# Optimization experiments

Hardware: AMD Instinct MI355X
Metric: run time of the kernel (lower is better)

## Reference

```python
import jax, jax.numpy as jnp
import numpy as np

N_NODES, N_EDGES, DIM = 50000, 800000, 128


def setup_inputs() -> dict:
    key = jax.random.key(0)
    ks = jax.random.split(key, 16)
    s = 1.0 / np.sqrt(DIM)
    inp = {
        "x": jax.random.normal(ks[0], (N_NODES, DIM), dtype=jnp.float32),
        "edge_index": jax.random.randint(ks[1], (2, N_EDGES), 0, N_NODES, dtype=jnp.int64),
    }
    # 3 GIN layers, each with a 2-layer MLP (Linear-ReLU-Linear)
    for i in range(3):
        inp[f"w1_{i}"] = jax.random.normal(ks[2 + 4 * i], (DIM, DIM), dtype=jnp.float32) * s
        inp[f"b1_{i}"] = jnp.zeros((DIM,), dtype=jnp.float32)
        inp[f"w2_{i}"] = jax.random.normal(ks[3 + 4 * i], (DIM, DIM), dtype=jnp.float32) * s
        inp[f"b2_{i}"] = jnp.zeros((DIM,), dtype=jnp.float32)
    inp["wh"] = jax.random.normal(ks[14], (DIM, DIM), dtype=jnp.float32) * s
    inp["bh"] = jnp.zeros((DIM,), dtype=jnp.float32)
    return inp


def _gin_layer(h, src, dst, w1, b1, w2, b2, residual):
    # message passing: gather x[src], scatter-add at dst (aggr='sum')
    neigh = jax.ops.segment_sum(h[src], dst, num_segments=h.shape[0])
    out = h + neigh  # (1 + eps) * x + neigh, eps = 0
    out = jnp.maximum(out @ w1 + b1, 0.0) @ w2 + b2  # MLP (dropout p=0)
    if residual:  # res_fc is Identity since in_dim == out_dim
        out = out + h
    return out


def reference(x, edge_index, w1_0, b1_0, w2_0, b2_0, w1_1, b1_1, w2_1, b2_1,
              w1_2, b1_2, w2_2, b2_2, wh, bh):
    src, dst = edge_index[0], edge_index[1]
    h = x
    h = _gin_layer(h, src, dst, w1_0, b1_0, w2_0, b2_0, residual=True)
    h = _gin_layer(h, src, dst, w1_1, b1_1, w2_1, b2_1, residual=True)
    # last layer: encoding=False -> no residual
    h = _gin_layer(h, src, dst, w1_2, b1_2, w2_2, b2_2, residual=False)
    # extra_output_fc head
    return h @ wh + bh
```

## Files before the change

kernel.cpp:

```cpp
#include <hip/hip_runtime.h>
#include <hip/hip_fp16.h>

#define N_NODES 50000
#define N_EDGES 800000
#define DIM 128
#define FEAT_ELEMS (N_NODES * DIM)
#define STRIDE 64
#define NB 391
#define BCAP 3072

typedef __attribute__((ext_vector_type(8))) _Float16 f16x8;
typedef __attribute__((ext_vector_type(4))) float f32x4;
typedef __attribute__((ext_vector_type(2))) float f32x2;

#define MFMA_F16 __builtin_amdgcn_mfma_f32_16x16x32_f16


__global__ __launch_bounds__(256) void prep_combo_kernel(
    const float* __restrict__ w0, const float* __restrict__ w1,
    const float* __restrict__ w2, const float* __restrict__ w3,
    const float* __restrict__ w4, const float* __restrict__ w5,
    const float* __restrict__ w6, __half* __restrict__ dst,
    const float* __restrict__ x, __half* __restrict__ hm,
    unsigned char* __restrict__ qx, unsigned char* __restrict__ q1,
    unsigned char* __restrict__ q0, int* __restrict__ gcnt) {
    const int b = blockIdx.x;
    if (b < 112) {
        const int wsel = b >> 4;
        const int chunk = b & 15;
        const float* W;
        switch (wsel) {
            case 0: W = w0; break;
            case 1: W = w1; break;
            case 2: W = w2; break;
            case 3: W = w3; break;
            case 4: W = w4; break;
            case 5: W = w5; break;
            default: W = w6; break;
        }
        __half* d = dst + (size_t)wsel * 16384;
        int idx = chunk * 1024 + threadIdx.x;
#pragma unroll
        for (int t = 0; t < 4; ++t, idx += 256) {
            int k = idx >> 7, n = idx & 127;
            int ks = k >> 5, q = (k >> 3) & 3, j = k & 7;
            int ct = n >> 4, c = n & 15;
            int lane = q * 16 + c;
            int base = ((ks * 8 + ct) * 64 + lane) * 8 + j;
            d[base] = __float2half(W[idx]);
        }
    } else if (b < 1136) {
        int i = (b - 112) * 256 + threadIdx.x;
        const int stride = 1024 * 256;
        const int n4 = FEAT_ELEMS / 4;
        for (; i < n4; i += stride) {
            float4 v = ((const float4*)x)[i];
            __half2 h0 = __floats2half2_rn(v.x, v.y);
            __half2 h1 = __floats2half2_rn(v.z, v.w);
            uint2 u;
            u.x = *(unsigned*)&h0;
            u.y = *(unsigned*)&h1;
            ((uint2*)hm)[i] = u;
            int p = __builtin_amdgcn_cvt_pk_fp8_f32(v.x, v.y, 0, false);
            p = __builtin_amdgcn_cvt_pk_fp8_f32(v.z, v.w, p, true);
            ((int*)qx)[i] = p;
        }
    } else {
        for (int i = threadIdx.x; i < NB; i += 256) gcnt[i] = 0;
        if (threadIdx.x < 32) {
            ((unsigned*)(qx + FEAT_ELEMS))[threadIdx.x] = 0;
            ((unsigned*)(q1 + FEAT_ELEMS))[threadIdx.x] = 0;
            ((unsigned*)(q0 + FEAT_ELEMS))[threadIdx.x] = 0;
        }
    }
}


__global__ __launch_bounds__(256) void bucket_kernel(const int* __restrict__ ei,
                                                     int* __restrict__ gcnt,
                                                     long long* __restrict__ ebuf) {
    __shared__ int hist[NB];
    __shared__ int base[NB];
    __shared__ int sh_is64;
    const int tid = threadIdx.x;
    for (int i = tid; i < NB; i += 256) hist[i] = 0;
    if (tid == 0) {
        int o = 0;
        for (int i = 1; i < 64; i += 2) o |= ei[i];
        sh_is64 = (o == 0) ? 1 : 0;
    }
    __syncthreads();
    const int e0 = blockIdx.x * 2048;
    const int is64 = sh_is64;
    int sv[8], dv[8];
    int nl = 0;
#pragma unroll
    for (int k = 0; k < 8; ++k) {
        int e = e0 + k * 256 + tid;
        if (e < N_EDGES) {
            int s = is64 ? ei[2 * e] : ei[e];
            int d = is64 ? ei[2 * (N_EDGES + e)] : ei[N_EDGES + e];
            sv[nl] = s;
            dv[nl] = d;
            atomicAdd(&hist[d >> 7], 1);
            ++nl;
        }
    }
    __syncthreads();
    for (int i = tid; i < NB; i += 256) {
        int h = hist[i];
        base[i] = h ? atomicAdd(&gcnt[i], h) : 0;
    }
    __syncthreads();
    for (int i = tid; i < NB; i += 256) hist[i] = 0;
    __syncthreads();
    for (int k = 0; k < nl; ++k) {
        int b = dv[k] >> 7;
        int r = base[b] + atomicAdd(&hist[b], 1);
        if (r < BCAP)
            ebuf[(size_t)b * BCAP + r] = ((long long)sv[k] << 32) | (unsigned)dv[k];
    }
}


__global__ __launch_bounds__(256) void build_kernel(const int* __restrict__ gcnt,
                                                    const long long* __restrict__ ebuf,
                                                    int* __restrict__ cnt,
                                                    int* __restrict__ col_idx) {
    __shared__ int cur[128];
    const int b = blockIdx.x;
    const int tid = threadIdx.x;
    if (tid < 128) cur[tid] = 0;
    __syncthreads();
    int n = gcnt[b];
    if (n > BCAP) n = BCAP;
    const long long* eb = ebuf + (size_t)b * BCAP;
    for (int i = tid; i < n; i += 256) {
        long long p = eb[i];
        int d = (int)(p & 0xFFFFFFFFll);
        int s = (int)(p >> 32);
        int slot = atomicAdd(&cur[d & 127], 1);
        if (slot < STRIDE) col_idx[d * STRIDE + slot] = s;
    }
    __syncthreads();
    int node = b * 128 + tid;
    if (tid < 128 && node < N_NODES) {
        int c = cur[tid];
        if (c > STRIDE) c = STRIDE;
        const int p = (c + 7) & ~7;
        for (int s = c; s < p; ++s) col_idx[node * STRIDE + s] = N_NODES;
        cnt[node] = p;
    }
}


template <bool LAST>
__global__ __launch_bounds__(128, 4) void gin_layer_kernel(
    const __half* __restrict__ Hs,
    const unsigned char* __restrict__ Qm,
    const int* __restrict__ cnt,
    const int* __restrict__ col_idx,
    const __half* __restrict__ W1f,
    const __half* __restrict__ W2f,
    const __half* __restrict__ Whf,
    const float* __restrict__ b1,
    const float* __restrict__ b2,
    const float* __restrict__ bh,
    __half* __restrict__ Hout,
    unsigned char* __restrict__ Qout,
    float* __restrict__ Cout) {
    __shared__ __align__(16) __half tl[2048];
    __shared__ __align__(16) __half ul[2048];
    const int tid = threadIdx.x;
    const int lane = tid & 63;
    const int wid = tid >> 6;
    const int c = lane & 15;
    const int q = lane >> 4;
    const int R = blockIdx.x * 16;

    {
        const int g = tid >> 4;
        const int d0 = (tid & 15) * 8;
#define ACCQ(U)                                                             \
    {                                                                       \
        f32x2 g0 = __builtin_amdgcn_cvt_pk_f32_fp8((int)(U).x, false);      \
        f32x2 g1 = __builtin_amdgcn_cvt_pk_f32_fp8((int)(U).x, true);       \
        f32x2 g2 = __builtin_amdgcn_cvt_pk_f32_fp8((int)(U).y, false);      \
        f32x2 g3 = __builtin_amdgcn_cvt_pk_f32_fp8((int)(U).y, true);       \
        acc[0] += g0.x; acc[1] += g0.y; acc[2] += g1.x; acc[3] += g1.y;     \
        acc[4] += g2.x; acc[5] += g2.y; acc[6] += g3.x; acc[7] += g3.y;     \
    }
#pragma unroll
        for (int it = 0; it < 2; ++it) {
            const int rl = it * 8 + g;
            const size_t grow = (size_t)(R + rl);
            float acc[8];
            {
                uint4 sv = *(const uint4*)(Hs + grow * DIM + d0);
                const __half2* sp = (const __half2*)&sv;
                float2 s0 = __half22float2(sp[0]), s1 = __half22float2(sp[1]);
                float2 s2 = __half22float2(sp[2]), s3 = __half22float2(sp[3]);
                acc[0] = s0.x; acc[1] = s0.y; acc[2] = s1.x; acc[3] = s1.y;
                acc[4] = s2.x; acc[5] = s2.y; acc[6] = s3.x; acc[7] = s3.y;
            }
            const int d = cnt[grow];
            const int* ci = col_idx + grow * STRIDE;
            for (int j = 0; j < d; j += 8) {
                int4 ia = *(const int4*)(ci + j);
                int4 ib = *(const int4*)(ci + j + 4);
                uint2 u0 = *(const uint2*)(Qm + (size_t)ia.x * DIM + d0);
                uint2 u1 = *(const uint2*)(Qm + (size_t)ia.y * DIM + d0);
                uint2 u2 = *(const uint2*)(Qm + (size_t)ia.z * DIM + d0);
                uint2 u3 = *(const uint2*)(Qm + (size_t)ia.w * DIM + d0);
                uint2 u4 = *(const uint2*)(Qm + (size_t)ib.x * DIM + d0);
                uint2 u5 = *(const uint2*)(Qm + (size_t)ib.y * DIM + d0);
                uint2 u6 = *(const uint2*)(Qm + (size_t)ib.z * DIM + d0);
                uint2 u7 = *(const uint2*)(Qm + (size_t)ib.w * DIM + d0);
                ACCQ(u0) ACCQ(u1) ACCQ(u2) ACCQ(u3)
                ACCQ(u4) ACCQ(u5) ACCQ(u6) ACCQ(u7)
            }
            uint4 o;
            __half2* op = (__half2*)&o;
            op[0] = __floats2half2_rn(acc[0], acc[1]);
            op[1] = __floats2half2_rn(acc[2], acc[3]);
            op[2] = __floats2half2_rn(acc[4], acc[5]);
            op[3] = __floats2half2_rn(acc[6], acc[7]);
            *(uint4*)&tl[rl * 128 + (d0 ^ ((rl & 7) << 3))] = o;
        }
#undef ACCQ
    }
    __syncthreads();

    f16x8 a[4];
#pragma unroll
    for (int ks = 0; ks < 4; ++ks)
        a[ks] = *(const f16x8*)&tl[c * 128 + ((ks * 32 + q * 8) ^ ((c & 7) << 3))];

    f32x4 acc1[4];
#pragma unroll
    for (int t = 0; t < 4; ++t) acc1[t] = (f32x4){0.f, 0.f, 0.f, 0.f};
#pragma unroll
    for (int ks = 0; ks < 4; ++ks) {
#pragma unroll
        for (int t = 0; t < 4; ++t) {
            const int ctg = wid * 4 + t;
            f16x8 b = *(const f16x8*)(W1f + (ks * 8 + ctg) * 512 + lane * 8);
            acc1[t] = MFMA_F16(a[ks], b, acc1[t], 0, 0, 0);
        }
    }

#pragma unroll
    for (int t = 0; t < 4; ++t) {
        const int col = (wid * 4 + t) * 16 + c;
        const float bv = b1[col];
#pragma unroll
        for (int rr = 0; rr < 4; ++rr) {
            const int rl = q * 4 + rr;
            ul[rl * 128 + (col ^ ((rl & 7) << 3))] =
                __float2half(fmaxf(acc1[t][rr] + bv, 0.f));
        }
    }
    __syncthreads();

    f32x4 acc2[4];
#pragma unroll
    for (int t = 0; t < 4; ++t) acc2[t] = (f32x4){0.f, 0.f, 0.f, 0.f};
#pragma unroll
    for (int ks = 0; ks < 4; ++ks) {
        f16x8 ua = *(const f16x8*)&ul[c * 128 + ((ks * 32 + q * 8) ^ ((c & 7) << 3))];
#pragma unroll
        for (int t = 0; t < 4; ++t) {
            const int ctg = wid * 4 + t;
            f16x8 b = *(const f16x8*)(W2f + (ks * 8 + ctg) * 512 + lane * 8);
            acc2[t] = MFMA_F16(ua, b, acc2[t], 0, 0, 0);
        }
    }

#pragma unroll
    for (int t = 0; t < 4; ++t) {
        const int col = (wid * 4 + t) * 16 + c;
        const float bv = b2[col];
#pragma unroll
        for (int rr = 0; rr < 4; ++rr) {
            const int rl = q * 4 + rr;
            tl[rl * 128 + (col ^ (q << 4))] = __float2half(acc2[t][rr] + bv);
        }
    }
    __syncthreads();

    if (!LAST) {
        const int row2 = tid >> 3;
        const int cb = (tid & 7) * 8;
        const size_t grow = (size_t)(R + row2);
#pragma unroll
        for (int k = 0; k < 2; ++k) {
            const int c0 = cb + k * 64;
            uint4 hv = *(uint4*)&tl[row2 * 128 + (c0 ^ ((row2 >> 2) << 4))];
            const __half2* hp = (const __half2*)&hv;
            float2 t0 = __half22float2(hp[0]), t1 = __half22float2(hp[1]);
            float2 t2 = __half22float2(hp[2]), t3 = __half22float2(hp[3]);
            float f0 = t0.x, f1 = t0.y, f2 = t1.x, f3 = t1.y;
            float f4 = t2.x, f5 = t2.y, f6 = t3.x, f7 = t3.y;
            {
                uint4 rv = *(const uint4*)(Hs + grow * DIM + c0);
                const __half2* rp = (const __half2*)&rv;
                float2 r0 = __half22float2(rp[0]), r1 = __half22float2(rp[1]);
                float2 r2 = __half22float2(rp[2]), r3 = __half22float2(rp[3]);
                f0 += r0.x; f1 += r0.y; f2 += r1.x; f3 += r1.y;
                f4 += r2.x; f5 += r2.y; f6 += r3.x; f7 += r3.y;
            }
            uint4 ov;
            __half2* op = (__half2*)&ov;
            op[0] = __floats2half2_rn(f0, f1);
            op[1] = __floats2half2_rn(f2, f3);
            op[2] = __floats2half2_rn(f4, f5);
            op[3] = __floats2half2_rn(f6, f7);
            *(uint4*)(Hout + grow * DIM + c0) = ov;
            int q0 = __builtin_amdgcn_cvt_pk_fp8_f32(f0, f1, 0, false);
            q0 = __builtin_amdgcn_cvt_pk_fp8_f32(f2, f3, q0, true);
            int q1 = __builtin_amdgcn_cvt_pk_fp8_f32(f4, f5, 0, false);
            q1 = __builtin_amdgcn_cvt_pk_fp8_f32(f6, f7, q1, true);
            uint2 qv;
            qv.x = (unsigned)q0;
            qv.y = (unsigned)q1;
            *(uint2*)(Qout + grow * DIM + c0) = qv;
        }
    } else {
        f32x4 acc3[4];
#pragma unroll
        for (int t = 0; t < 4; ++t) acc3[t] = (f32x4){0.f, 0.f, 0.f, 0.f};
#pragma unroll
        for (int ks = 0; ks < 4; ++ks) {
            f16x8 ha =
                *(const f16x8*)&tl[c * 128 + ((ks * 32 + q * 8) ^ ((c >> 2) << 4))];
#pragma unroll
            for (int t = 0; t < 4; ++t) {
                const int ctg = wid * 4 + t;
                f16x8 b = *(const f16x8*)(Whf + (ks * 8 + ctg) * 512 + lane * 8);
                acc3[t] = MFMA_F16(ha, b, acc3[t], 0, 0, 0);
            }
        }
#pragma unroll
        for (int t = 0; t < 4; ++t) {
            const int col = (wid * 4 + t) * 16 + c;
            const float bv = bh[col];
#pragma unroll
            for (int rr = 0; rr < 4; ++rr) {
                const int row = R + q * 4 + rr;
                Cout[(size_t)row * DIM + col] = acc3[t][rr] + bv;
            }
        }
    }
}


extern "C" void kernel_launch(void* const* d_in, const int* in_sizes, int n_in,
                              void* d_out, int out_size, void* d_ws, size_t ws_size,
                              hipStream_t stream) {
    const float* x = (const float*)d_in[0];
    const int* ei = (const int*)d_in[1];
    const float* w1[3] = {(const float*)d_in[2], (const float*)d_in[6], (const float*)d_in[10]};
    const float* b1[3] = {(const float*)d_in[3], (const float*)d_in[7], (const float*)d_in[11]};
    const float* w2[3] = {(const float*)d_in[4], (const float*)d_in[8], (const float*)d_in[12]};
    const float* b2[3] = {(const float*)d_in[5], (const float*)d_in[9], (const float*)d_in[13]};
    const float* wh = (const float*)d_in[14];
    const float* bh = (const float*)d_in[15];
    float* out = (float*)d_out;

    char* ws = (char*)d_ws;
    const size_t HFEAT = (size_t)FEAT_ELEMS * sizeof(__half);
    const size_t QFEAT = (size_t)FEAT_ELEMS + 256;
    size_t off = 0;
    int* cnt = (int*)(ws + off);                         off += 200704;
    int* col_idx = (int*)(ws + off);                     off += (size_t)N_NODES * STRIDE * 4;
    int* gcnt = (int*)(ws + off);                        off += 4096;
    __half* Wf = (__half*)(ws + off);                    off += 7 * 32768;
    long long* ebuf = (long long*)(ws + off);            off += (size_t)NB * BCAP * 8;
    __half* HMx = (__half*)(ws + off);                   off += HFEAT;
    __half* HM1 = (__half*)(ws + off);                   off += HFEAT;
    __half* HM0 = (__half*)(ws + off);                   off += HFEAT;
    unsigned char* Qx = (unsigned char*)(ws + off);      off += QFEAT;
    unsigned char* Q1 = (unsigned char*)(ws + off);      off += QFEAT;
    unsigned char* Q0 = (unsigned char*)(ws + off);      off += QFEAT;

    const int GIN_BLKS = N_NODES / 16;

    prep_combo_kernel<<<1137, 256, 0, stream>>>(w1[0], w2[0], w1[1], w2[1], w1[2], w2[2],
                                                wh, Wf, x, HMx, Qx, Q1, Q0, gcnt);
    bucket_kernel<<<NB, 256, 0, stream>>>(ei, gcnt, ebuf);
    build_kernel<<<NB, 256, 0, stream>>>(gcnt, ebuf, cnt, col_idx);

#define WF(i) (Wf + (size_t)(i) * 16384)

    gin_layer_kernel<false><<<GIN_BLKS, 128, 0, stream>>>(
        HMx, Qx, cnt, col_idx, WF(0), WF(1), nullptr, b1[0], b2[0], nullptr,
        HM1, Q1, nullptr);

    gin_layer_kernel<false><<<GIN_BLKS, 128, 0, stream>>>(
        HM1, Q1, cnt, col_idx, WF(2), WF(3), nullptr, b1[1], b2[1], nullptr,
        HM0, Q0, nullptr);

    gin_layer_kernel<true><<<GIN_BLKS, 128, 0, stream>>>(
        HM0, Q0, cnt, col_idx, WF(4), WF(5), WF(6), b1[2], b2[2], bh,
        nullptr, nullptr, out);
#undef WF
}
```

Baseline: 216.2 us.

## Split fp8 feature table into column halves and fuse bucketing into prep

Stores the fp8 gather table as two 64-column halves so each aggregation pass gathers from a 3.2MB array that is more likely to stay cache-resident. The gather runs two passes, one per half, with 8 threads per row instead of 16. Edge bucketing is folded into the prep kernel, and the gcnt reset moves to a memset, which removes one kernel launch. The cost is reading col_idx twice per row and a memset node. The gcnt reset must finish before the fused kernel's atomics, which stream ordering guarantees.

```diff
diff --git a/kernel.cpp b/kernel.cpp
--- a/kernel.cpp
+++ b/kernel.cpp
@@ -16,15 +16,22 @@
 #define MFMA_F16 __builtin_amdgcn_mfma_f32_16x16x32_f16
 
 
-__global__ __launch_bounds__(256) void prep_combo_kernel(
+__global__ __launch_bounds__(256) void prep_bucket_kernel(
     const float* __restrict__ w0, const float* __restrict__ w1,
     const float* __restrict__ w2, const float* __restrict__ w3,
     const float* __restrict__ w4, const float* __restrict__ w5,
     const float* __restrict__ w6, __half* __restrict__ dst,
     const float* __restrict__ x, __half* __restrict__ hm,
-    unsigned char* __restrict__ qx, unsigned char* __restrict__ q1,
-    unsigned char* __restrict__ q0, int* __restrict__ gcnt) {
+    unsigned char* __restrict__ qxlo, unsigned char* __restrict__ qxhi,
+    unsigned char* __restrict__ q1lo, unsigned char* __restrict__ q1hi,
+    unsigned char* __restrict__ q0lo, unsigned char* __restrict__ q0hi,
+    const int* __restrict__ ei, int* __restrict__ gcnt,
+    long long* __restrict__ ebuf) {
+    __shared__ int hist[NB];
+    __shared__ int base[NB];
+    __shared__ int sh_is64;
     const int b = blockIdx.x;
+    const int tid = threadIdx.x;
     if (b < 112) {
         const int wsel = b >> 4;
         const int chunk = b & 15;
@@ -39,18 +46,18 @@
             default: W = w6; break;
         }
         __half* d = dst + (size_t)wsel * 16384;
-        int idx = chunk * 1024 + threadIdx.x;
+        int idx = chunk * 1024 + tid;
 #pragma unroll
         for (int t = 0; t < 4; ++t, idx += 256) {
             int k = idx >> 7, n = idx & 127;
             int ks = k >> 5, q = (k >> 3) & 3, j = k & 7;
             int ct = n >> 4, c = n & 15;
             int lane = q * 16 + c;
-            int base = ((ks * 8 + ct) * 64 + lane) * 8 + j;
-            d[base] = __float2half(W[idx]);
+            int bas = ((ks * 8 + ct) * 64 + lane) * 8 + j;
+            d[bas] = __float2half(W[idx]);
         }
     } else if (b < 1136) {
-        int i = (b - 112) * 256 + threadIdx.x;
+        int i = (b - 112) * 256 + tid;
         const int stride = 1024 * 256;
         const int n4 = FEAT_ELEMS / 4;
         for (; i < n4; i += stride) {
@@ -63,62 +70,58 @@
             ((uint2*)hm)[i] = u;
             int p = __builtin_amdgcn_cvt_pk_fp8_f32(v.x, v.y, 0, false);
             p = __builtin_amdgcn_cvt_pk_fp8_f32(v.z, v.w, p, true);
-            ((int*)qx)[i] = p;
+            const int node = i >> 5;
+            const int within = (i & 31) * 4;
+            if (within < 64)
+                *(int*)(qxlo + (size_t)node * 64 + within) = p;
+            else
+                *(int*)(qxhi + (size_t)node * 64 + (within - 64)) = p;
+        }
+    } else if (b < 1527) {
+        for (int i = tid; i < NB; i += 256) hist[i] = 0;
+        if (tid == 0) {
+            int o = 0;
+            for (int i = 1; i < 64; i += 2) o |= ei[i];
+            sh_is64 = (o == 0) ? 1 : 0;
+        }
+        __syncthreads();
+        const int e0 = (b - 1136) * 2048;
+        const int is64 = sh_is64;
+        int sv[8], dv[8];
+        int nl = 0;
+#pragma unroll
+        for (int k = 0; k < 8; ++k) {
+            int e = e0 + k * 256 + tid;
+            if (e < N_EDGES) {
+                int s = is64 ? ei[2 * e] : ei[e];
+                int d = is64 ? ei[2 * (N_EDGES + e)] : ei[N_EDGES + e];
+                sv[nl] = s;
+                dv[nl] = d;
+                atomicAdd(&hist[d >> 7], 1);
+                ++nl;
+            }
+        }
+        __syncthreads();
+        for (int i = tid; i < NB; i += 256) {
+            int h = hist[i];
+            base[i] = h ? atomicAdd(&gcnt[i], h) : 0;
+        }
+        __syncthreads();
+        for (int i = tid; i < NB; i += 256) hist[i] = 0;
+        __syncthreads();
+        for (int k = 0; k < nl; ++k) {
+            int bb = dv[k] >> 7;
+            int r = base[bb] + atomicAdd(&hist[bb], 1);
+            if (r < BCAP)
+                ebuf[(size_t)bb * BCAP + r] = ((long long)sv[k] << 32) | (unsigned)dv[k];
         }
     } else {
-        for (int i = threadIdx.x; i < NB; i += 256) gcnt[i] = 0;
-        if (threadIdx.x < 32) {
-            ((unsigned*)(qx + FEAT_ELEMS))[threadIdx.x] = 0;
-            ((unsigned*)(q1 + FEAT_ELEMS))[threadIdx.x] = 0;
-            ((unsigned*)(q0 + FEAT_ELEMS))[threadIdx.x] = 0;
-        }
-    }
-}
-
-
-__global__ __launch_bounds__(256) void bucket_kernel(const int* __restrict__ ei,
-                                                     int* __restrict__ gcnt,
-                                                     long long* __restrict__ ebuf) {
-    __shared__ int hist[NB];
-    __shared__ int base[NB];
-    __shared__ int sh_is64;
-    const int tid = threadIdx.x;
-    for (int i = tid; i < NB; i += 256) hist[i] = 0;
-    if (tid == 0) {
-        int o = 0;
-        for (int i = 1; i < 64; i += 2) o |= ei[i];
-        sh_is64 = (o == 0) ? 1 : 0;
-    }
-    __syncthreads();
-    const int e0 = blockIdx.x * 2048;
-    const int is64 = sh_is64;
-    int sv[8], dv[8];
-    int nl = 0;
-#pragma unroll
-    for (int k = 0; k < 8; ++k) {
-        int e = e0 + k * 256 + tid;
-        if (e < N_EDGES) {
-            int s = is64 ? ei[2 * e] : ei[e];
-            int d = is64 ? ei[2 * (N_EDGES + e)] : ei[N_EDGES + e];
-            sv[nl] = s;
-            dv[nl] = d;
-            atomicAdd(&hist[d >> 7], 1);
-            ++nl;
-        }
-    }
-    __syncthreads();
-    for (int i = tid; i < NB; i += 256) {
-        int h = hist[i];
-        base[i] = h ? atomicAdd(&gcnt[i], h) : 0;
-    }
-    __syncthreads();
-    for (int i = tid; i < NB; i += 256) hist[i] = 0;
-    __syncthreads();
-    for (int k = 0; k < nl; ++k) {
-        int b = dv[k] >> 7;
-        int r = base[b] + atomicAdd(&hist[b], 1);
-        if (r < BCAP)
-            ebuf[(size_t)b * BCAP + r] = ((long long)sv[k] << 32) | (unsigned)dv[k];
+        if (tid < 16) *(unsigned*)(qxlo + (size_t)N_NODES * 64 + tid * 4) = 0;
+        else if (tid < 32) *(unsigned*)(qxhi + (size_t)N_NODES * 64 + (tid - 16) * 4) = 0;
+        else if (tid < 48) *(unsigned*)(q1lo + (size_t)N_NODES * 64 + (tid - 32) * 4) = 0;
+        else if (tid < 64) *(unsigned*)(q1hi + (size_t)N_NODES * 64 + (tid - 48) * 4) = 0;
+        else if (tid < 80) *(unsigned*)(q0lo + (size_t)N_NODES * 64 + (tid - 64) * 4) = 0;
+        else if (tid < 96) *(unsigned*)(q0hi + (size_t)N_NODES * 64 + (tid - 80) * 4) = 0;
     }
 }
 
@@ -157,7 +160,8 @@
 template <bool LAST>
 __global__ __launch_bounds__(128, 4) void gin_layer_kernel(
     const __half* __restrict__ Hs,
-    const unsigned char* __restrict__ Qm,
+    const unsigned char* __restrict__ Qlo,
+    const unsigned char* __restrict__ Qhi,
     const int* __restrict__ cnt,
     const int* __restrict__ col_idx,
     const __half* __restrict__ W1f,
@@ -167,7 +171,8 @@
     const float* __restrict__ b2,
     const float* __restrict__ bh,
     __half* __restrict__ Hout,
-    unsigned char* __restrict__ Qout,
+    unsigned char* __restrict__ Qoutlo,
+    unsigned char* __restrict__ Qouthi,
     float* __restrict__ Cout) {
     __shared__ __align__(16) __half tl[2048];
     __shared__ __align__(16) __half ul[2048];
@@ -179,8 +184,12 @@
     const int R = blockIdx.x * 16;
 
     {
-        const int g = tid >> 4;
-        const int d0 = (tid & 15) * 8;
+        const int row = tid >> 3;
+        const int d0b = (tid & 7) * 8;
+        const size_t grow = (size_t)(R + row);
+        const int d = cnt[grow];
+        const int* ci = col_idx + grow * STRIDE;
+        const int swz = (row & 7) << 3;
 #define ACCQ(U)                                                             \
     {                                                                       \
         f32x2 g0 = __builtin_amdgcn_cvt_pk_f32_fp8((int)(U).x, false);      \
@@ -190,43 +199,42 @@
         acc[0] += g0.x; acc[1] += g0.y; acc[2] += g1.x; acc[3] += g1.y;     \
         acc[4] += g2.x; acc[5] += g2.y; acc[6] += g3.x; acc[7] += g3.y;     \
     }
-#pragma unroll
-        for (int it = 0; it < 2; ++it) {
-            const int rl = it * 8 + g;
-            const size_t grow = (size_t)(R + rl);
-            float acc[8];
-            {
-                uint4 sv = *(const uint4*)(Hs + grow * DIM + d0);
-                const __half2* sp = (const __half2*)&sv;
-                float2 s0 = __half22float2(sp[0]), s1 = __half22float2(sp[1]);
-                float2 s2 = __half22float2(sp[2]), s3 = __half22float2(sp[3]);
-                acc[0] = s0.x; acc[1] = s0.y; acc[2] = s1.x; acc[3] = s1.y;
-                acc[4] = s2.x; acc[5] = s2.y; acc[6] = s3.x; acc[7] = s3.y;
-            }
-            const int d = cnt[grow];
-            const int* ci = col_idx + grow * STRIDE;
-            for (int j = 0; j < d; j += 8) {
-                int4 ia = *(const int4*)(ci + j);
-                int4 ib = *(const int4*)(ci + j + 4);
-                uint2 u0 = *(const uint2*)(Qm + (size_t)ia.x * DIM + d0);
-                uint2 u1 = *(const uint2*)(Qm + (size_t)ia.y * DIM + d0);
-                uint2 u2 = *(const uint2*)(Qm + (size_t)ia.z * DIM + d0);
-                uint2 u3 = *(const uint2*)(Qm + (size_t)ia.w * DIM + d0);
-                uint2 u4 = *(const uint2*)(Qm + (size_t)ib.x * DIM + d0);
-                uint2 u5 = *(const uint2*)(Qm + (size_t)ib.y * DIM + d0);
-                uint2 u6 = *(const uint2*)(Qm + (size_t)ib.z * DIM + d0);
-                uint2 u7 = *(const uint2*)(Qm + (size_t)ib.w * DIM + d0);
-                ACCQ(u0) ACCQ(u1) ACCQ(u2) ACCQ(u3)
-                ACCQ(u4) ACCQ(u5) ACCQ(u6) ACCQ(u7)
-            }
-            uint4 o;
-            __half2* op = (__half2*)&o;
-            op[0] = __floats2half2_rn(acc[0], acc[1]);
-            op[1] = __floats2half2_rn(acc[2], acc[3]);
-            op[2] = __floats2half2_rn(acc[4], acc[5]);
-            op[3] = __floats2half2_rn(acc[6], acc[7]);
-            *(uint4*)&tl[rl * 128 + (d0 ^ ((rl & 7) << 3))] = o;
-        }
+#define GATHER_PASS(QP, CB)                                                     \
+    {                                                                           \
+        float acc[8];                                                           \
+        {                                                                       \
+            uint4 sv = *(const uint4*)(Hs + grow * DIM + (CB) + d0b);           \
+            const __half2* sp = (const __half2*)&sv;                            \
+            float2 s0 = __half22float2(sp[0]), s1 = __half22float2(sp[1]);      \
+            float2 s2 = __half22float2(sp[2]), s3 = __half22float2(sp[3]);      \
+            acc[0] = s0.x; acc[1] = s0.y; acc[2] = s1.x; acc[3] = s1.y;         \
+            acc[4] = s2.x; acc[5] = s2.y; acc[6] = s3.x; acc[7] = s3.y;         \
+        }                                                                       \
+        for (int j = 0; j < d; j += 8) {                                        \
+            int4 ia = *(const int4*)(ci + j);                                   \
+            int4 ib = *(const int4*)(ci + j + 4);                               \
+            uint2 u0 = *(const uint2*)((QP) + (size_t)ia.x * 64 + d0b);         \
+            uint2 u1 = *(const uint2*)((QP) + (size_t)ia.y * 64 + d0b);         \
+            uint2 u2 = *(const uint2*)((QP) + (size_t)ia.z * 64 + d0b);         \
+            uint2 u3 = *(const uint2*)((QP) + (size_t)ia.w * 64 + d0b);         \
+            uint2 u4 = *(const uint2*)((QP) + (size_t)ib.x * 64 + d0b);         \
+            uint2 u5 = *(const uint2*)((QP) + (size_t)ib.y * 64 + d0b);         \
+            uint2 u6 = *(const uint2*)((QP) + (size_t)ib.z * 64 + d0b);         \
+            uint2 u7 = *(const uint2*)((QP) + (size_t)ib.w * 64 + d0b);         \
+            ACCQ(u0) ACCQ(u1) ACCQ(u2) ACCQ(u3)                                 \
+            ACCQ(u4) ACCQ(u5) ACCQ(u6) ACCQ(u7)                                 \
+        }                                                                       \
+        uint4 o;                                                                \
+        __half2* op = (__half2*)&o;                                             \
+        op[0] = __floats2half2_rn(acc[0], acc[1]);                              \
+        op[1] = __floats2half2_rn(acc[2], acc[3]);                              \
+        op[2] = __floats2half2_rn(acc[4], acc[5]);                              \
+        op[3] = __floats2half2_rn(acc[6], acc[7]);                              \
+        *(uint4*)&tl[row * 128 + (((CB) + d0b) ^ swz)] = o;                     \
+    }
+        GATHER_PASS(Qlo, 0)
+        GATHER_PASS(Qhi, 64)
+#undef GATHER_PASS
 #undef ACCQ
     }
     __syncthreads();
@@ -323,7 +331,10 @@
             uint2 qv;
             qv.x = (unsigned)q0;
             qv.y = (unsigned)q1;
-            *(uint2*)(Qout + grow * DIM + c0) = qv;
+            if (k == 0)
+                *(uint2*)(Qoutlo + grow * 64 + cb) = qv;
+            else
+                *(uint2*)(Qouthi + grow * 64 + cb) = qv;
         }
     } else {
         f32x4 acc3[4];
@@ -369,7 +380,7 @@
 
     char* ws = (char*)d_ws;
     const size_t HFEAT = (size_t)FEAT_ELEMS * sizeof(__half);
-    const size_t QFEAT = (size_t)FEAT_ELEMS + 256;
+    const size_t QH = (size_t)N_NODES * 64 + 64;
     size_t off = 0;
     int* cnt = (int*)(ws + off);                         off += 200704;
     int* col_idx = (int*)(ws + off);                     off += (size_t)N_NODES * STRIDE * 4;
@@ -379,29 +390,33 @@
     __half* HMx = (__half*)(ws + off);                   off += HFEAT;
     __half* HM1 = (__half*)(ws + off);                   off += HFEAT;
     __half* HM0 = (__half*)(ws + off);                   off += HFEAT;
-    unsigned char* Qx = (unsigned char*)(ws + off);      off += QFEAT;
-    unsigned char* Q1 = (unsigned char*)(ws + off);      off += QFEAT;
-    unsigned char* Q0 = (unsigned char*)(ws + off);      off += QFEAT;
+    unsigned char* Qxlo = (unsigned char*)(ws + off);    off += QH;
+    unsigned char* Qxhi = (unsigned char*)(ws + off);    off += QH;
+    unsigned char* Q1lo = (unsigned char*)(ws + off);    off += QH;
+    unsigned char* Q1hi = (unsigned char*)(ws + off);    off += QH;
+    unsigned char* Q0lo = (unsigned char*)(ws + off);    off += QH;
+    unsigned char* Q0hi = (unsigned char*)(ws + off);    off += QH;
 
     const int GIN_BLKS = N_NODES / 16;
 
-    prep_combo_kernel<<<1137, 256, 0, stream>>>(w1[0], w2[0], w1[1], w2[1], w1[2], w2[2],
-                                                wh, Wf, x, HMx, Qx, Q1, Q0, gcnt);
-    bucket_kernel<<<NB, 256, 0, stream>>>(ei, gcnt, ebuf);
+    (void)hipMemsetAsync(gcnt, 0, NB * sizeof(int), stream);
+    prep_bucket_kernel<<<1528, 256, 0, stream>>>(
+        w1[0], w2[0], w1[1], w2[1], w1[2], w2[2], wh, Wf, x, HMx,
+        Qxlo, Qxhi, Q1lo, Q1hi, Q0lo, Q0hi, ei, gcnt, ebuf);
     build_kernel<<<NB, 256, 0, stream>>>(gcnt, ebuf, cnt, col_idx);
 
 #define WF(i) (Wf + (size_t)(i) * 16384)
 
     gin_layer_kernel<false><<<GIN_BLKS, 128, 0, stream>>>(
-        HMx, Qx, cnt, col_idx, WF(0), WF(1), nullptr, b1[0], b2[0], nullptr,
-        HM1, Q1, nullptr);
+        HMx, Qxlo, Qxhi, cnt, col_idx, WF(0), WF(1), nullptr, b1[0], b2[0], nullptr,
+        HM1, Q1lo, Q1hi, nullptr);
 
     gin_layer_kernel<false><<<GIN_BLKS, 128, 0, stream>>>(
-        HM1, Q1, cnt, col_idx, WF(2), WF(3), nullptr, b1[1], b2[1], nullptr,
-        HM0, Q0, nullptr);
+        HM1, Q1lo, Q1hi, cnt, col_idx, WF(2), WF(3), nullptr, b1[1], b2[1], nullptr,
+        HM0, Q0lo, Q0hi, nullptr);
 
     gin_layer_kernel<true><<<GIN_BLKS, 128, 0, stream>>>(
-        HM0, Q0, cnt, col_idx, WF(4), WF(5), WF(6), b1[2], b2[2], bh,
-        nullptr, nullptr, out);
+        HM0, Q0lo, Q0hi, cnt, col_idx, WF(4), WF(5), WF(6), b1[2], b2[2], bh,
+        nullptr, nullptr, nullptr, out);
 #undef WF
 }
```

Result: slower. 224.0 us (+3.6%).
